# Kernel optimization log

Hardware: AMD Instinct MI355X
Metric: run time of the kernel (lower is better)

Reference implementation:

```python
import jax, jax.numpy as jnp
import numpy as np

EMBED = 1024
HEADS = 16
HEAD_DIM = EMBED // HEADS
SCALE = HEAD_DIM ** -0.5


def setup_inputs() -> dict:
    key = jax.random.key(0)
    ks = jax.random.split(key, 5)
    B, N = 2, 2048
    x = jax.random.normal(ks[0], (B, N, EMBED), dtype=jnp.float32)
    # qkv Linear: weight [3*EMBED, EMBED], bias [3*EMBED]
    w_qkv = jax.random.normal(ks[1], (3 * EMBED, EMBED), dtype=jnp.float32) * (EMBED ** -0.5)
    b_qkv = jnp.zeros((3 * EMBED,), dtype=jnp.float32)
    # proj Linear: weight [EMBED, EMBED], bias [EMBED]
    w_proj = jax.random.normal(ks[2], (EMBED, EMBED), dtype=jnp.float32) * (EMBED ** -0.5)
    b_proj = jnp.zeros((EMBED,), dtype=jnp.float32)
    return {"x": x, "w_qkv": w_qkv, "b_qkv": b_qkv, "w_proj": w_proj, "b_proj": b_proj}


def reference(x, w_qkv, b_qkv, w_proj, b_proj):
    B, N, _ = x.shape
    # QKV projection: [B, N, 3*EMBED]
    qkv = jnp.einsum('bnc,dc->bnd', x, w_qkv) + b_qkv
    qkv = qkv.reshape(B, N, 3, HEADS, HEAD_DIM).transpose(2, 0, 3, 1, 4)  # [3, B, H, N, Dh]
    q, k, v = qkv[0], qkv[1], qkv[2]
    # Explicit attention: matmul -> scale -> softmax -> matmul (eval mode, no dropout)
    attn = jnp.einsum('bhqd,bhkd->bhqk', q, k) * SCALE
    attn = jax.nn.softmax(attn, axis=-1)
    out = jnp.einsum('bhqk,bhkd->bhqd', attn, v)
    out = out.transpose(0, 2, 1, 3).reshape(B, N, EMBED)
    # Output projection (gamma1 is Identity; dropouts are zero in eval)
    out = jnp.einsum('bnc,dc->bnd', out, w_proj) + b_proj
    return out
```

## Files before the change

### kernel.cpp

```cpp
#include <hip/hip_runtime.h>
#include <stdint.h>

#define SEQ 2048

typedef __attribute__((ext_vector_type(8))) short bf16x8;
typedef __attribute__((ext_vector_type(4))) float f32x4;

typedef const __attribute__((address_space(1))) unsigned int GVT;
typedef __attribute__((address_space(3))) unsigned int LVT;

static __device__ __forceinline__ unsigned short f2bf(float f) {
  unsigned u = __builtin_bit_cast(unsigned, f);
  u += 0x7fffu + ((u >> 16) & 1u);
  return (unsigned short)(u >> 16);
}

static __device__ __forceinline__ unsigned pk_bf16(float lo, float hi) {
  unsigned r;
  asm("v_cvt_pk_bf16_f32 %0, %1, %2" : "=v"(r) : "v"(lo), "v"(hi));
  return r;
}

__global__ __launch_bounds__(256) void cvt_kernel(const float* __restrict__ src,
                                                  unsigned short* __restrict__ dst, int n4) {
  int i = blockIdx.x * 256 + threadIdx.x;
  const int stride = gridDim.x * 256;
  for (; i < n4; i += stride) {
    float4 v = reinterpret_cast<const float4*>(src)[i];
    ushort4 o;
    o.x = f2bf(v.x); o.y = f2bf(v.y); o.z = f2bf(v.z); o.w = f2bf(v.w);
    reinterpret_cast<ushort4*>(dst)[i] = o;
  }
}

__global__ __launch_bounds__(256, 2) void gemm_qkv_kernel(
    const unsigned short* __restrict__ A,
    const unsigned short* __restrict__ Bt,
    const float* __restrict__ bias,
    unsigned short* __restrict__ qb,
    unsigned short* __restrict__ kbuf,
    unsigned short* __restrict__ vtbuf) {
  __shared__ __align__(16) unsigned short As[2][128 * 32];
  __shared__ __align__(16) unsigned short Bs[2][128 * 32];
  const int tid = threadIdx.x;
  const int lane = tid & 63;
  const int wid = tid >> 6;
  const int wr = wid >> 1, wc = wid & 1;
  const int bm = blockIdx.y, bn = blockIdx.x;
  const int lr = lane & 15, hg = lane >> 4;

  f32x4 acc[4][4] = {};

  const int r0 = tid >> 2;
  const int c0 = (tid & 3) * 8;

  auto STAGE = [&](int b, int kt) {
    const unsigned short* ga0 = A + (size_t)(bm * 128 + r0) * 1024 + kt * 32 + c0;
    const unsigned short* ga1 = A + (size_t)(bm * 128 + r0 + 64) * 1024 + kt * 32 + c0;
    const unsigned short* gb0 = Bt + (size_t)(bn * 128 + r0) * 1024 + kt * 32 + c0;
    const unsigned short* gb1 = Bt + (size_t)(bn * 128 + r0 + 64) * 1024 + kt * 32 + c0;
    __builtin_amdgcn_global_load_lds((GVT*)ga0, (LVT*)&As[b][tid * 8], 16, 0, 0);
    __builtin_amdgcn_global_load_lds((GVT*)ga1, (LVT*)&As[b][(tid + 256) * 8], 16, 0, 0);
    __builtin_amdgcn_global_load_lds((GVT*)gb0, (LVT*)&Bs[b][tid * 8], 16, 0, 0);
    __builtin_amdgcn_global_load_lds((GVT*)gb1, (LVT*)&Bs[b][(tid + 256) * 8], 16, 0, 0);
  };

  STAGE(0, 0);
  int cur = 0;
  for (int kt = 0; kt < 32; ++kt) {
    __syncthreads();
    if (kt + 1 < 32) STAGE(cur ^ 1, kt + 1);
    bf16x8 af[4], bfr[4];
#pragma unroll
    for (int i = 0; i < 4; ++i) {
      af[i] = *reinterpret_cast<const bf16x8*>(&As[cur][(wr * 64 + i * 16 + lr) * 32 + hg * 8]);
      bfr[i] = *reinterpret_cast<const bf16x8*>(&Bs[cur][(wc * 64 + i * 16 + lr) * 32 + hg * 8]);
    }
#pragma unroll
    for (int i = 0; i < 4; ++i)
#pragma unroll
      for (int j = 0; j < 4; ++j)
        acc[i][j] = __builtin_amdgcn_mfma_f32_16x16x32_bf16(af[i], bfr[j], acc[i][j], 0, 0, 0);
    cur ^= 1;
  }

#pragma unroll
  for (int j = 0; j < 4; ++j) {
    const int col = bn * 128 + wc * 64 + j * 16 + lr;
    const float bv = bias[col];
    const int which = col >> 10;
    const int hh = (col >> 6) & 15;
    const int dh = col & 63;
    const float scl = which == 0 ? 0.18033688011112042f : 1.0f;
#pragma unroll
    for (int i = 0; i < 4; ++i) {
      if (which == 2) {
        const int row0 = bm * 128 + wr * 64 + i * 16 + hg * 4;
        const int b = row0 >> 11, n0 = row0 & 2047;
        ushort4 vv;
        vv.x = f2bf(acc[i][j][0] + bv);
        vv.y = f2bf(acc[i][j][1] + bv);
        vv.z = f2bf(acc[i][j][2] + bv);
        vv.w = f2bf(acc[i][j][3] + bv);
        *reinterpret_cast<ushort4*>(
            &vtbuf[((size_t)((b * 16 + hh) * 64 + dh)) * 2048 + n0]) = vv;
      } else {
        unsigned short* dst = which == 0 ? qb : kbuf;
#pragma unroll
        for (int r = 0; r < 4; ++r) {
          const int row = bm * 128 + wr * 64 + i * 16 + hg * 4 + r;
          const int b = row >> 11, n = row & 2047;
          dst[((size_t)((b * 16 + hh) * 2048 + n)) * 64 + dh] = f2bf((acc[i][j][r] + bv) * scl);
        }
      }
    }
  }
}

__global__ __launch_bounds__(256, 2) void gemm_proj_kernel(
    const unsigned short* __restrict__ A,
    const unsigned short* __restrict__ Bt,
    const float* __restrict__ bias,
    float* __restrict__ out) {
  __shared__ __align__(16) unsigned short As[2][128 * 32];
  __shared__ __align__(16) unsigned short Bs[2][128 * 32];
  const int tid = threadIdx.x;
  const int lane = tid & 63;
  const int wid = tid >> 6;
  const int wr = wid >> 1, wc = wid & 1;
  const int bm = blockIdx.y, bn = blockIdx.x;
  const int lr = lane & 15, hg = lane >> 4;

  f32x4 acc[4][4] = {};
  const int r0 = tid >> 2;
  const int c0 = (tid & 3) * 8;

  auto STAGE = [&](int b, int kt) {
    const unsigned short* ga0 = A + (size_t)(bm * 128 + r0) * 1024 + kt * 32 + c0;
    const unsigned short* ga1 = A + (size_t)(bm * 128 + r0 + 64) * 1024 + kt * 32 + c0;
    const unsigned short* gb0 = Bt + (size_t)(bn * 128 + r0) * 1024 + kt * 32 + c0;
    const unsigned short* gb1 = Bt + (size_t)(bn * 128 + r0 + 64) * 1024 + kt * 32 + c0;
    __builtin_amdgcn_global_load_lds((GVT*)ga0, (LVT*)&As[b][tid * 8], 16, 0, 0);
    __builtin_amdgcn_global_load_lds((GVT*)ga1, (LVT*)&As[b][(tid + 256) * 8], 16, 0, 0);
    __builtin_amdgcn_global_load_lds((GVT*)gb0, (LVT*)&Bs[b][tid * 8], 16, 0, 0);
    __builtin_amdgcn_global_load_lds((GVT*)gb1, (LVT*)&Bs[b][(tid + 256) * 8], 16, 0, 0);
  };

  STAGE(0, 0);
  int cur = 0;
  for (int kt = 0; kt < 32; ++kt) {
    __syncthreads();
    if (kt + 1 < 32) STAGE(cur ^ 1, kt + 1);
    bf16x8 af[4], bfr[4];
#pragma unroll
    for (int i = 0; i < 4; ++i) {
      af[i] = *reinterpret_cast<const bf16x8*>(&As[cur][(wr * 64 + i * 16 + lr) * 32 + hg * 8]);
      bfr[i] = *reinterpret_cast<const bf16x8*>(&Bs[cur][(wc * 64 + i * 16 + lr) * 32 + hg * 8]);
    }
#pragma unroll
    for (int i = 0; i < 4; ++i)
#pragma unroll
      for (int j = 0; j < 4; ++j)
        acc[i][j] = __builtin_amdgcn_mfma_f32_16x16x32_bf16(af[i], bfr[j], acc[i][j], 0, 0, 0);
    cur ^= 1;
  }

#pragma unroll
  for (int j = 0; j < 4; ++j) {
    const int col = bn * 128 + wc * 64 + j * 16 + lr;
    const float bv = bias[col];
#pragma unroll
    for (int i = 0; i < 4; ++i)
#pragma unroll
      for (int r = 0; r < 4; ++r) {
        const int row = bm * 128 + wr * 64 + i * 16 + hg * 4 + r;
        out[(size_t)row * 1024 + col] = acc[i][j][r] + bv;
      }
  }
}

__global__ __launch_bounds__(256, 2) void attn_kernel(
    const unsigned short* __restrict__ qb,
    const unsigned short* __restrict__ kbuf,
    const unsigned short* __restrict__ vt,
    unsigned short* __restrict__ ao) {
  __shared__ __align__(16) unsigned short Ks[2][64 * 64];
  __shared__ __align__(16) unsigned short Vs[2][64 * 64];
  __shared__ __align__(16) unsigned short Ps[4][32][88];
  const int tid = threadIdx.x;
  const int lane = tid & 63;
  const int wid = tid >> 6;
  const int lr = lane & 15;
  const int hg = lane >> 4;
  const int lin = blockIdx.y * 16 + blockIdx.x;
  const int wg = (lin & 7) * 64 + (lin >> 3);
  const int qt = wg & 15;
  const int bh = wg >> 4;
  const size_t hbase = (size_t)bh * SEQ * 64;

  bf16x8 qf[2][2];
#pragma unroll
  for (int m = 0; m < 2; ++m) {
    const unsigned short* qp =
        qb + hbase + (size_t)(qt * 128 + wid * 32 + m * 16 + lr) * 64 + hg * 8;
    qf[m][0] = *reinterpret_cast<const bf16x8*>(qp);
    qf[m][1] = *reinterpret_cast<const bf16x8*>(qp + 32);
  }

  f32x4 accO[2][4] = {};
  float m_run[2] = {-1e30f, -1e30f};
  float l_run[2] = {0.0f, 0.0f};

  auto STAGE = [&](int b, int kt) {
#pragma unroll
    for (int c = 0; c < 2; ++c) {
      const int t = tid + c * 256;
      const int row = t >> 3;
      const int sw = ((t & 7) ^ (row & 7)) * 8;
      const unsigned short* gk = kbuf + hbase + (size_t)(kt * 64 + row) * 64 + sw;
      __builtin_amdgcn_global_load_lds((GVT*)gk, (LVT*)&Ks[b][t * 8], 16, 0, 0);
      const unsigned short* gv = vt + hbase + (size_t)row * 2048 + kt * 64 + sw;
      __builtin_amdgcn_global_load_lds((GVT*)gv, (LVT*)&Vs[b][t * 8], 16, 0, 0);
    }
  };

  STAGE(0, 0);
  int cur = 0;
  const int sw0 = (hg ^ (lr & 7)) * 8;
  const int sw1 = ((hg + 4) ^ (lr & 7)) * 8;

  for (int kt = 0; kt < 32; ++kt) {
    __syncthreads();
    if (kt + 1 < 32) STAGE(cur ^ 1, kt + 1);

    f32x4 accT[2][4] = {};
#pragma unroll
    for (int j = 0; j < 4; ++j) {
      const bf16x8 kf0 = *reinterpret_cast<const bf16x8*>(&Ks[cur][(j * 16 + lr) * 64 + sw0]);
      const bf16x8 kf1 = *reinterpret_cast<const bf16x8*>(&Ks[cur][(j * 16 + lr) * 64 + sw1]);
      accT[0][j] = __builtin_amdgcn_mfma_f32_16x16x32_bf16(kf0, qf[0][0], accT[0][j], 0, 0, 0);
      accT[0][j] = __builtin_amdgcn_mfma_f32_16x16x32_bf16(kf1, qf[0][1], accT[0][j], 0, 0, 0);
      accT[1][j] = __builtin_amdgcn_mfma_f32_16x16x32_bf16(kf0, qf[1][0], accT[1][j], 0, 0, 0);
      accT[1][j] = __builtin_amdgcn_mfma_f32_16x16x32_bf16(kf1, qf[1][1], accT[1][j], 0, 0, 0);
    }

#pragma unroll
    for (int m = 0; m < 2; ++m) {
      float mt = accT[m][0][0];
#pragma unroll
      for (int j = 0; j < 4; ++j)
#pragma unroll
        for (int r = 0; r < 4; ++r) mt = fmaxf(mt, accT[m][j][r]);
      mt = fmaxf(mt, __shfl_xor(mt, 16));
      mt = fmaxf(mt, __shfl_xor(mt, 32));
      if (__any(mt > m_run[m] + 8.0f)) {
        const float mnew = fmaxf(m_run[m], mt);
        const float crr = __builtin_amdgcn_exp2f(m_run[m] - mnew);
        m_run[m] = mnew;
        l_run[m] *= crr;
#pragma unroll
        for (int jd = 0; jd < 4; ++jd)
#pragma unroll
          for (int r = 0; r < 4; ++r) accO[m][jd][r] *= crr;
      }
      float ps = 0.0f;
#pragma unroll
      for (int j = 0; j < 4; ++j) {
        const float p0 = __builtin_amdgcn_exp2f(accT[m][j][0] - m_run[m]);
        const float p1 = __builtin_amdgcn_exp2f(accT[m][j][1] - m_run[m]);
        const float p2 = __builtin_amdgcn_exp2f(accT[m][j][2] - m_run[m]);
        const float p3 = __builtin_amdgcn_exp2f(accT[m][j][3] - m_run[m]);
        ps += (p0 + p1) + (p2 + p3);
        uint2 w;
        w.x = pk_bf16(p0, p1);
        w.y = pk_bf16(p2, p3);
        *reinterpret_cast<uint2*>(&Ps[wid][m * 16 + lr][j * 16 + hg * 4]) = w;
      }
      ps += __shfl_xor(ps, 16);
      ps += __shfl_xor(ps, 32);
      l_run[m] += ps;
    }

    bf16x8 pB[2][2];
#pragma unroll
    for (int m = 0; m < 2; ++m) {
      pB[m][0] = *reinterpret_cast<const bf16x8*>(&Ps[wid][m * 16 + lr][hg * 8]);
      pB[m][1] = *reinterpret_cast<const bf16x8*>(&Ps[wid][m * 16 + lr][32 + hg * 8]);
    }
#pragma unroll
    for (int jd = 0; jd < 4; ++jd) {
      const bf16x8 v0 = *reinterpret_cast<const bf16x8*>(&Vs[cur][(jd * 16 + lr) * 64 + sw0]);
      const bf16x8 v1 = *reinterpret_cast<const bf16x8*>(&Vs[cur][(jd * 16 + lr) * 64 + sw1]);
      accO[0][jd] = __builtin_amdgcn_mfma_f32_16x16x32_bf16(v0, pB[0][0], accO[0][jd], 0, 0, 0);
      accO[0][jd] = __builtin_amdgcn_mfma_f32_16x16x32_bf16(v1, pB[0][1], accO[0][jd], 0, 0, 0);
      accO[1][jd] = __builtin_amdgcn_mfma_f32_16x16x32_bf16(v0, pB[1][0], accO[1][jd], 0, 0, 0);
      accO[1][jd] = __builtin_amdgcn_mfma_f32_16x16x32_bf16(v1, pB[1][1], accO[1][jd], 0, 0, 0);
    }
    cur ^= 1;
  }

  const int b = bh >> 4, hh = bh & 15;
#pragma unroll
  for (int m = 0; m < 2; ++m) {
    const float invl = 1.0f / l_run[m];
    const int qrow = qt * 128 + wid * 32 + m * 16 + lr;
    unsigned short* dst = ao + (size_t)(b * 2048 + qrow) * 1024 + hh * 64;
#pragma unroll
    for (int jd = 0; jd < 4; ++jd) {
      uint2 o;
      o.x = pk_bf16(accO[m][jd][0] * invl, accO[m][jd][1] * invl);
      o.y = pk_bf16(accO[m][jd][2] * invl, accO[m][jd][3] * invl);
      *reinterpret_cast<uint2*>(dst + jd * 16 + hg * 4) = o;
    }
  }
}

extern "C" void kernel_launch(void* const* d_in, const int* in_sizes, int n_in,
                              void* d_out, int out_size, void* d_ws, size_t ws_size,
                              hipStream_t stream) {
  const float* x = (const float*)d_in[0];
  const float* w_qkv = (const float*)d_in[1];
  const float* b_qkv = (const float*)d_in[2];
  const float* w_proj = (const float*)d_in[3];
  const float* b_proj = (const float*)d_in[4];
  float* out = (float*)d_out;
  char* ws = (char*)d_ws;
  unsigned short* x_bf = (unsigned short*)(ws);
  unsigned short* ao_bf = (unsigned short*)(ws);
  unsigned short* wq_bf = (unsigned short*)(ws + (8ull << 20));
  unsigned short* wp_bf = (unsigned short*)(ws + (14ull << 20));
  unsigned short* q_bf = (unsigned short*)(ws + (16ull << 20));
  unsigned short* k_bf = (unsigned short*)(ws + (24ull << 20));
  unsigned short* vt_bf = (unsigned short*)(ws + (32ull << 20));

  cvt_kernel<<<1024, 256, 0, stream>>>(x, x_bf, 4096 * 1024 / 4);
  cvt_kernel<<<1024, 256, 0, stream>>>(w_qkv, wq_bf, 3072 * 1024 / 4);
  cvt_kernel<<<512, 256, 0, stream>>>(w_proj, wp_bf, 1024 * 1024 / 4);
  gemm_qkv_kernel<<<dim3(24, 32), 256, 0, stream>>>(x_bf, wq_bf, b_qkv, q_bf, k_bf, vt_bf);
  attn_kernel<<<dim3(16, 32), 256, 0, stream>>>(q_bf, k_bf, vt_bf, ao_bf);
  gemm_proj_kernel<<<dim3(8, 32), 256, 0, stream>>>(ao_bf, wp_bf, b_proj, out);
}
```

Baseline: 136.5 us.

## Fuse conversion kernels, remap GEMM tiles, and load attention K/V directly into registers

Merges the three fp32-to-bf16 conversion launches into one kernel. Remaps GEMM workgroup indices with an XCD-aware swizzle to improve L2 locality. Raises wave priority around the MFMA blocks with s_setprio. The attention kernel drops its LDS K/V staging: each wave reads its K and V fragments straight from global memory into registers, prefetching the next tile, and the max reduction is restructured into a tree. This removes barriers and LDS traffic, but every wave now loads K/V separately from global/L2 instead of sharing them through LDS.

```diff
diff --git a/kernel.cpp b/kernel.cpp
--- a/kernel.cpp
+++ b/kernel.cpp
@@ -21,15 +21,24 @@
   return r;
 }
 
-__global__ __launch_bounds__(256) void cvt_kernel(const float* __restrict__ src,
-                                                  unsigned short* __restrict__ dst, int n4) {
+__global__ __launch_bounds__(256) void cvt3_kernel(
+    const float* __restrict__ s0, unsigned short* __restrict__ d0, int n0,
+    const float* __restrict__ s1, unsigned short* __restrict__ d1, int n1,
+    const float* __restrict__ s2, unsigned short* __restrict__ d2, int n2) {
   int i = blockIdx.x * 256 + threadIdx.x;
   const int stride = gridDim.x * 256;
-  for (; i < n4; i += stride) {
-    float4 v = reinterpret_cast<const float4*>(src)[i];
+  const int total = n0 + n1 + n2;
+  for (; i < total; i += stride) {
+    const float* s;
+    unsigned short* d;
+    int k;
+    if (i < n0) { s = s0; d = d0; k = i; }
+    else if (i < n0 + n1) { s = s1; d = d1; k = i - n0; }
+    else { s = s2; d = d2; k = i - n0 - n1; }
+    float4 v = reinterpret_cast<const float4*>(s)[k];
     ushort4 o;
     o.x = f2bf(v.x); o.y = f2bf(v.y); o.z = f2bf(v.z); o.w = f2bf(v.w);
-    reinterpret_cast<ushort4*>(dst)[i] = o;
+    reinterpret_cast<ushort4*>(d)[k] = o;
   }
 }
 
@@ -46,7 +55,9 @@
   const int lane = tid & 63;
   const int wid = tid >> 6;
   const int wr = wid >> 1, wc = wid & 1;
-  const int bm = blockIdx.y, bn = blockIdx.x;
+  const int lin = blockIdx.y * 24 + blockIdx.x;
+  const int wg = (lin & 7) * 96 + (lin >> 3);
+  const int bm = wg / 24, bn = wg % 24;
   const int lr = lane & 15, hg = lane >> 4;
 
   f32x4 acc[4][4] = {};
@@ -76,11 +87,13 @@
       af[i] = *reinterpret_cast<const bf16x8*>(&As[cur][(wr * 64 + i * 16 + lr) * 32 + hg * 8]);
       bfr[i] = *reinterpret_cast<const bf16x8*>(&Bs[cur][(wc * 64 + i * 16 + lr) * 32 + hg * 8]);
     }
+    __builtin_amdgcn_s_setprio(1);
 #pragma unroll
     for (int i = 0; i < 4; ++i)
 #pragma unroll
       for (int j = 0; j < 4; ++j)
         acc[i][j] = __builtin_amdgcn_mfma_f32_16x16x32_bf16(af[i], bfr[j], acc[i][j], 0, 0, 0);
+    __builtin_amdgcn_s_setprio(0);
     cur ^= 1;
   }
 
@@ -128,7 +141,9 @@
   const int lane = tid & 63;
   const int wid = tid >> 6;
   const int wr = wid >> 1, wc = wid & 1;
-  const int bm = blockIdx.y, bn = blockIdx.x;
+  const int lin = blockIdx.y * 8 + blockIdx.x;
+  const int wg = (lin & 7) * 32 + (lin >> 3);
+  const int bm = wg / 8, bn = wg % 8;
   const int lr = lane & 15, hg = lane >> 4;
 
   f32x4 acc[4][4] = {};
@@ -157,11 +172,13 @@
       af[i] = *reinterpret_cast<const bf16x8*>(&As[cur][(wr * 64 + i * 16 + lr) * 32 + hg * 8]);
       bfr[i] = *reinterpret_cast<const bf16x8*>(&Bs[cur][(wc * 64 + i * 16 + lr) * 32 + hg * 8]);
     }
+    __builtin_amdgcn_s_setprio(1);
 #pragma unroll
     for (int i = 0; i < 4; ++i)
 #pragma unroll
       for (int j = 0; j < 4; ++j)
         acc[i][j] = __builtin_amdgcn_mfma_f32_16x16x32_bf16(af[i], bfr[j], acc[i][j], 0, 0, 0);
+    __builtin_amdgcn_s_setprio(0);
     cur ^= 1;
   }
 
@@ -184,8 +201,6 @@
     const unsigned short* __restrict__ kbuf,
     const unsigned short* __restrict__ vt,
     unsigned short* __restrict__ ao) {
-  __shared__ __align__(16) unsigned short Ks[2][64 * 64];
-  __shared__ __align__(16) unsigned short Vs[2][64 * 64];
   __shared__ __align__(16) unsigned short Ps[4][32][88];
   const int tid = threadIdx.x;
   const int lane = tid & 63;
@@ -207,50 +222,49 @@
     qf[m][1] = *reinterpret_cast<const bf16x8*>(qp + 32);
   }
 
+  bf16x8 kf[4][2];
+  bf16x8 vf[4][2];
+  const unsigned short* kb0 = kbuf + hbase + (size_t)(lr)*64 + hg * 8;
+  const unsigned short* vb0 = vt + hbase + (size_t)(lr)*2048 + hg * 8;
+#pragma unroll
+  for (int j = 0; j < 4; ++j) {
+    kf[j][0] = *reinterpret_cast<const bf16x8*>(kb0 + (size_t)(j * 16) * 64);
+    kf[j][1] = *reinterpret_cast<const bf16x8*>(kb0 + (size_t)(j * 16) * 64 + 32);
+    vf[j][0] = *reinterpret_cast<const bf16x8*>(vb0 + (size_t)(j * 16) * 2048);
+    vf[j][1] = *reinterpret_cast<const bf16x8*>(vb0 + (size_t)(j * 16) * 2048 + 32);
+  }
+
   f32x4 accO[2][4] = {};
   float m_run[2] = {-1e30f, -1e30f};
   float l_run[2] = {0.0f, 0.0f};
 
-  auto STAGE = [&](int b, int kt) {
-#pragma unroll
-    for (int c = 0; c < 2; ++c) {
-      const int t = tid + c * 256;
-      const int row = t >> 3;
-      const int sw = ((t & 7) ^ (row & 7)) * 8;
-      const unsigned short* gk = kbuf + hbase + (size_t)(kt * 64 + row) * 64 + sw;
-      __builtin_amdgcn_global_load_lds((GVT*)gk, (LVT*)&Ks[b][t * 8], 16, 0, 0);
-      const unsigned short* gv = vt + hbase + (size_t)row * 2048 + kt * 64 + sw;
-      __builtin_amdgcn_global_load_lds((GVT*)gv, (LVT*)&Vs[b][t * 8], 16, 0, 0);
-    }
-  };
-
-  STAGE(0, 0);
-  int cur = 0;
-  const int sw0 = (hg ^ (lr & 7)) * 8;
-  const int sw1 = ((hg + 4) ^ (lr & 7)) * 8;
-
   for (int kt = 0; kt < 32; ++kt) {
-    __syncthreads();
-    if (kt + 1 < 32) STAGE(cur ^ 1, kt + 1);
+    const int ktn = kt < 31 ? kt + 1 : 31;
 
     f32x4 accT[2][4] = {};
+    __builtin_amdgcn_s_setprio(1);
 #pragma unroll
     for (int j = 0; j < 4; ++j) {
-      const bf16x8 kf0 = *reinterpret_cast<const bf16x8*>(&Ks[cur][(j * 16 + lr) * 64 + sw0]);
-      const bf16x8 kf1 = *reinterpret_cast<const bf16x8*>(&Ks[cur][(j * 16 + lr) * 64 + sw1]);
-      accT[0][j] = __builtin_amdgcn_mfma_f32_16x16x32_bf16(kf0, qf[0][0], accT[0][j], 0, 0, 0);
-      accT[0][j] = __builtin_amdgcn_mfma_f32_16x16x32_bf16(kf1, qf[0][1], accT[0][j], 0, 0, 0);
-      accT[1][j] = __builtin_amdgcn_mfma_f32_16x16x32_bf16(kf0, qf[1][0], accT[1][j], 0, 0, 0);
-      accT[1][j] = __builtin_amdgcn_mfma_f32_16x16x32_bf16(kf1, qf[1][1], accT[1][j], 0, 0, 0);
+      accT[0][j] = __builtin_amdgcn_mfma_f32_16x16x32_bf16(kf[j][0], qf[0][0], accT[0][j], 0, 0, 0);
+      accT[0][j] = __builtin_amdgcn_mfma_f32_16x16x32_bf16(kf[j][1], qf[0][1], accT[0][j], 0, 0, 0);
+      accT[1][j] = __builtin_amdgcn_mfma_f32_16x16x32_bf16(kf[j][0], qf[1][0], accT[1][j], 0, 0, 0);
+      accT[1][j] = __builtin_amdgcn_mfma_f32_16x16x32_bf16(kf[j][1], qf[1][1], accT[1][j], 0, 0, 0);
+    }
+    __builtin_amdgcn_s_setprio(0);
+
+#pragma unroll
+    for (int j = 0; j < 4; ++j) {
+      kf[j][0] = *reinterpret_cast<const bf16x8*>(kb0 + (size_t)(ktn * 64 + j * 16) * 64);
+      kf[j][1] = *reinterpret_cast<const bf16x8*>(kb0 + (size_t)(ktn * 64 + j * 16) * 64 + 32);
     }
 
 #pragma unroll
     for (int m = 0; m < 2; ++m) {
-      float mt = accT[m][0][0];
-#pragma unroll
-      for (int j = 0; j < 4; ++j)
-#pragma unroll
-        for (int r = 0; r < 4; ++r) mt = fmaxf(mt, accT[m][j][r]);
+      float t0 = fmaxf(fmaxf(accT[m][0][0], accT[m][0][1]), fmaxf(accT[m][0][2], accT[m][0][3]));
+      float t1 = fmaxf(fmaxf(accT[m][1][0], accT[m][1][1]), fmaxf(accT[m][1][2], accT[m][1][3]));
+      float t2 = fmaxf(fmaxf(accT[m][2][0], accT[m][2][1]), fmaxf(accT[m][2][2], accT[m][2][3]));
+      float t3 = fmaxf(fmaxf(accT[m][3][0], accT[m][3][1]), fmaxf(accT[m][3][2], accT[m][3][3]));
+      float mt = fmaxf(fmaxf(t0, t1), fmaxf(t2, t3));
       mt = fmaxf(mt, __shfl_xor(mt, 16));
       mt = fmaxf(mt, __shfl_xor(mt, 32));
       if (__any(mt > m_run[m] + 8.0f)) {
@@ -263,19 +277,21 @@
 #pragma unroll
           for (int r = 0; r < 4; ++r) accO[m][jd][r] *= crr;
       }
-      float ps = 0.0f;
+      float ps0 = 0.f, ps1 = 0.f;
 #pragma unroll
       for (int j = 0; j < 4; ++j) {
         const float p0 = __builtin_amdgcn_exp2f(accT[m][j][0] - m_run[m]);
         const float p1 = __builtin_amdgcn_exp2f(accT[m][j][1] - m_run[m]);
         const float p2 = __builtin_amdgcn_exp2f(accT[m][j][2] - m_run[m]);
         const float p3 = __builtin_amdgcn_exp2f(accT[m][j][3] - m_run[m]);
-        ps += (p0 + p1) + (p2 + p3);
+        ps0 += (p0 + p1);
+        ps1 += (p2 + p3);
         uint2 w;
         w.x = pk_bf16(p0, p1);
         w.y = pk_bf16(p2, p3);
         *reinterpret_cast<uint2*>(&Ps[wid][m * 16 + lr][j * 16 + hg * 4]) = w;
       }
+      float ps = ps0 + ps1;
       ps += __shfl_xor(ps, 16);
       ps += __shfl_xor(ps, 32);
       l_run[m] += ps;
@@ -287,16 +303,21 @@
       pB[m][0] = *reinterpret_cast<const bf16x8*>(&Ps[wid][m * 16 + lr][hg * 8]);
       pB[m][1] = *reinterpret_cast<const bf16x8*>(&Ps[wid][m * 16 + lr][32 + hg * 8]);
     }
+    __builtin_amdgcn_s_setprio(1);
 #pragma unroll
     for (int jd = 0; jd < 4; ++jd) {
-      const bf16x8 v0 = *reinterpret_cast<const bf16x8*>(&Vs[cur][(jd * 16 + lr) * 64 + sw0]);
-      const bf16x8 v1 = *reinterpret_cast<const bf16x8*>(&Vs[cur][(jd * 16 + lr) * 64 + sw1]);
-      accO[0][jd] = __builtin_amdgcn_mfma_f32_16x16x32_bf16(v0, pB[0][0], accO[0][jd], 0, 0, 0);
-      accO[0][jd] = __builtin_amdgcn_mfma_f32_16x16x32_bf16(v1, pB[0][1], accO[0][jd], 0, 0, 0);
-      accO[1][jd] = __builtin_amdgcn_mfma_f32_16x16x32_bf16(v0, pB[1][0], accO[1][jd], 0, 0, 0);
-      accO[1][jd] = __builtin_amdgcn_mfma_f32_16x16x32_bf16(v1, pB[1][1], accO[1][jd], 0, 0, 0);
-    }
-    cur ^= 1;
+      accO[0][jd] = __builtin_amdgcn_mfma_f32_16x16x32_bf16(vf[jd][0], pB[0][0], accO[0][jd], 0, 0, 0);
+      accO[0][jd] = __builtin_amdgcn_mfma_f32_16x16x32_bf16(vf[jd][1], pB[0][1], accO[0][jd], 0, 0, 0);
+      accO[1][jd] = __builtin_amdgcn_mfma_f32_16x16x32_bf16(vf[jd][0], pB[1][0], accO[1][jd], 0, 0, 0);
+      accO[1][jd] = __builtin_amdgcn_mfma_f32_16x16x32_bf16(vf[jd][1], pB[1][1], accO[1][jd], 0, 0, 0);
+    }
+    __builtin_amdgcn_s_setprio(0);
+
+#pragma unroll
+    for (int jd = 0; jd < 4; ++jd) {
+      vf[jd][0] = *reinterpret_cast<const bf16x8*>(vb0 + (size_t)(jd * 16) * 2048 + ktn * 64);
+      vf[jd][1] = *reinterpret_cast<const bf16x8*>(vb0 + (size_t)(jd * 16) * 2048 + ktn * 64 + 32);
+    }
   }
 
   const int b = bh >> 4, hh = bh & 15;
@@ -333,9 +354,9 @@
   unsigned short* k_bf = (unsigned short*)(ws + (24ull << 20));
   unsigned short* vt_bf = (unsigned short*)(ws + (32ull << 20));
 
-  cvt_kernel<<<1024, 256, 0, stream>>>(x, x_bf, 4096 * 1024 / 4);
-  cvt_kernel<<<1024, 256, 0, stream>>>(w_qkv, wq_bf, 3072 * 1024 / 4);
-  cvt_kernel<<<512, 256, 0, stream>>>(w_proj, wp_bf, 1024 * 1024 / 4);
+  cvt3_kernel<<<2048, 256, 0, stream>>>(x, x_bf, 4096 * 1024 / 4,
+                                        w_qkv, wq_bf, 3072 * 1024 / 4,
+                                        w_proj, wp_bf, 1024 * 1024 / 4);
   gemm_qkv_kernel<<<dim3(24, 32), 256, 0, stream>>>(x_bf, wq_bf, b_qkv, q_bf, k_bf, vt_bf);
   attn_kernel<<<dim3(16, 32), 256, 0, stream>>>(q_bf, k_bf, vt_bf, ao_bf);
   gemm_proj_kernel<<<dim3(8, 32), 256, 0, stream>>>(ao_bf, wp_bf, b_proj, out);
```

Result: slower. 184.9 us (+35.5%).

## Fuse conversions, remap GEMM blocks, add setprio, and pass P via permlane swaps

Applied to the files above, without the earlier changes.

The three fp32-to-bf16 conversion launches become a single kernel. Both GEMMs remap block indices so consecutive workgroups spread across XCDs. s_setprio is raised around the MFMA bursts in the GEMMs and the attention kernel. The attention kernel drops the shared-memory round trip for the P tile and instead rearranges packed bf16 probabilities across lanes with v_permlane32/16_swap, which removes LDS writes and reads but depends on the lane mapping being exactly right.

```diff
diff --git a/kernel.cpp b/kernel.cpp
--- a/kernel.cpp
+++ b/kernel.cpp
@@ -5,6 +5,7 @@
 
 typedef __attribute__((ext_vector_type(8))) short bf16x8;
 typedef __attribute__((ext_vector_type(4))) float f32x4;
+typedef __attribute__((ext_vector_type(4))) int i32x4;
 
 typedef const __attribute__((address_space(1))) unsigned int GVT;
 typedef __attribute__((address_space(3))) unsigned int LVT;
@@ -21,15 +22,24 @@
   return r;
 }
 
-__global__ __launch_bounds__(256) void cvt_kernel(const float* __restrict__ src,
-                                                  unsigned short* __restrict__ dst, int n4) {
+__global__ __launch_bounds__(256) void cvt3_kernel(
+    const float* __restrict__ s0, unsigned short* __restrict__ d0, int n0,
+    const float* __restrict__ s1, unsigned short* __restrict__ d1, int n1,
+    const float* __restrict__ s2, unsigned short* __restrict__ d2, int n2) {
   int i = blockIdx.x * 256 + threadIdx.x;
   const int stride = gridDim.x * 256;
-  for (; i < n4; i += stride) {
-    float4 v = reinterpret_cast<const float4*>(src)[i];
+  const int total = n0 + n1 + n2;
+  for (; i < total; i += stride) {
+    const float* s;
+    unsigned short* d;
+    int k;
+    if (i < n0) { s = s0; d = d0; k = i; }
+    else if (i < n0 + n1) { s = s1; d = d1; k = i - n0; }
+    else { s = s2; d = d2; k = i - n0 - n1; }
+    float4 v = reinterpret_cast<const float4*>(s)[k];
     ushort4 o;
     o.x = f2bf(v.x); o.y = f2bf(v.y); o.z = f2bf(v.z); o.w = f2bf(v.w);
-    reinterpret_cast<ushort4*>(dst)[i] = o;
+    reinterpret_cast<ushort4*>(d)[k] = o;
   }
 }
 
@@ -46,7 +56,9 @@
   const int lane = tid & 63;
   const int wid = tid >> 6;
   const int wr = wid >> 1, wc = wid & 1;
-  const int bm = blockIdx.y, bn = blockIdx.x;
+  const int lin = blockIdx.y * 24 + blockIdx.x;
+  const int wg = (lin & 7) * 96 + (lin >> 3);
+  const int bm = wg / 24, bn = wg % 24;
   const int lr = lane & 15, hg = lane >> 4;
 
   f32x4 acc[4][4] = {};
@@ -76,11 +88,13 @@
       af[i] = *reinterpret_cast<const bf16x8*>(&As[cur][(wr * 64 + i * 16 + lr) * 32 + hg * 8]);
       bfr[i] = *reinterpret_cast<const bf16x8*>(&Bs[cur][(wc * 64 + i * 16 + lr) * 32 + hg * 8]);
     }
+    __builtin_amdgcn_s_setprio(1);
 #pragma unroll
     for (int i = 0; i < 4; ++i)
 #pragma unroll
       for (int j = 0; j < 4; ++j)
         acc[i][j] = __builtin_amdgcn_mfma_f32_16x16x32_bf16(af[i], bfr[j], acc[i][j], 0, 0, 0);
+    __builtin_amdgcn_s_setprio(0);
     cur ^= 1;
   }
 
@@ -128,7 +142,9 @@
   const int lane = tid & 63;
   const int wid = tid >> 6;
   const int wr = wid >> 1, wc = wid & 1;
-  const int bm = blockIdx.y, bn = blockIdx.x;
+  const int lin = blockIdx.y * 8 + blockIdx.x;
+  const int wg = (lin & 7) * 32 + (lin >> 3);
+  const int bm = wg / 8, bn = wg % 8;
   const int lr = lane & 15, hg = lane >> 4;
 
   f32x4 acc[4][4] = {};
@@ -157,11 +173,13 @@
       af[i] = *reinterpret_cast<const bf16x8*>(&As[cur][(wr * 64 + i * 16 + lr) * 32 + hg * 8]);
       bfr[i] = *reinterpret_cast<const bf16x8*>(&Bs[cur][(wc * 64 + i * 16 + lr) * 32 + hg * 8]);
     }
+    __builtin_amdgcn_s_setprio(1);
 #pragma unroll
     for (int i = 0; i < 4; ++i)
 #pragma unroll
       for (int j = 0; j < 4; ++j)
         acc[i][j] = __builtin_amdgcn_mfma_f32_16x16x32_bf16(af[i], bfr[j], acc[i][j], 0, 0, 0);
+    __builtin_amdgcn_s_setprio(0);
     cur ^= 1;
   }
 
@@ -186,7 +204,6 @@
     unsigned short* __restrict__ ao) {
   __shared__ __align__(16) unsigned short Ks[2][64 * 64];
   __shared__ __align__(16) unsigned short Vs[2][64 * 64];
-  __shared__ __align__(16) unsigned short Ps[4][32][88];
   const int tid = threadIdx.x;
   const int lane = tid & 63;
   const int wid = tid >> 6;
@@ -234,6 +251,7 @@
     if (kt + 1 < 32) STAGE(cur ^ 1, kt + 1);
 
     f32x4 accT[2][4] = {};
+    __builtin_amdgcn_s_setprio(1);
 #pragma unroll
     for (int j = 0; j < 4; ++j) {
       const bf16x8 kf0 = *reinterpret_cast<const bf16x8*>(&Ks[cur][(j * 16 + lr) * 64 + sw0]);
@@ -243,14 +261,16 @@
       accT[1][j] = __builtin_amdgcn_mfma_f32_16x16x32_bf16(kf0, qf[1][0], accT[1][j], 0, 0, 0);
       accT[1][j] = __builtin_amdgcn_mfma_f32_16x16x32_bf16(kf1, qf[1][1], accT[1][j], 0, 0, 0);
     }
-
+    __builtin_amdgcn_s_setprio(0);
+
+    bf16x8 pB[2][2];
 #pragma unroll
     for (int m = 0; m < 2; ++m) {
-      float mt = accT[m][0][0];
-#pragma unroll
-      for (int j = 0; j < 4; ++j)
-#pragma unroll
-        for (int r = 0; r < 4; ++r) mt = fmaxf(mt, accT[m][j][r]);
+      float t0 = fmaxf(fmaxf(accT[m][0][0], accT[m][0][1]), fmaxf(accT[m][0][2], accT[m][0][3]));
+      float t1 = fmaxf(fmaxf(accT[m][1][0], accT[m][1][1]), fmaxf(accT[m][1][2], accT[m][1][3]));
+      float t2 = fmaxf(fmaxf(accT[m][2][0], accT[m][2][1]), fmaxf(accT[m][2][2], accT[m][2][3]));
+      float t3 = fmaxf(fmaxf(accT[m][3][0], accT[m][3][1]), fmaxf(accT[m][3][2], accT[m][3][3]));
+      float mt = fmaxf(fmaxf(t0, t1), fmaxf(t2, t3));
       mt = fmaxf(mt, __shfl_xor(mt, 16));
       mt = fmaxf(mt, __shfl_xor(mt, 32));
       if (__any(mt > m_run[m] + 8.0f)) {
@@ -263,30 +283,37 @@
 #pragma unroll
           for (int r = 0; r < 4; ++r) accO[m][jd][r] *= crr;
       }
-      float ps = 0.0f;
+      unsigned w[4][2];
+      float ps0 = 0.f, ps1 = 0.f;
 #pragma unroll
       for (int j = 0; j < 4; ++j) {
         const float p0 = __builtin_amdgcn_exp2f(accT[m][j][0] - m_run[m]);
         const float p1 = __builtin_amdgcn_exp2f(accT[m][j][1] - m_run[m]);
         const float p2 = __builtin_amdgcn_exp2f(accT[m][j][2] - m_run[m]);
         const float p3 = __builtin_amdgcn_exp2f(accT[m][j][3] - m_run[m]);
-        ps += (p0 + p1) + (p2 + p3);
-        uint2 w;
-        w.x = pk_bf16(p0, p1);
-        w.y = pk_bf16(p2, p3);
-        *reinterpret_cast<uint2*>(&Ps[wid][m * 16 + lr][j * 16 + hg * 4]) = w;
-      }
+        ps0 += (p0 + p1);
+        ps1 += (p2 + p3);
+        w[j][0] = pk_bf16(p0, p1);
+        w[j][1] = pk_bf16(p2, p3);
+      }
+      float ps = ps0 + ps1;
       ps += __shfl_xor(ps, 16);
       ps += __shfl_xor(ps, 32);
       l_run[m] += ps;
-    }
-
-    bf16x8 pB[2][2];
-#pragma unroll
-    for (int m = 0; m < 2; ++m) {
-      pB[m][0] = *reinterpret_cast<const bf16x8*>(&Ps[wid][m * 16 + lr][hg * 8]);
-      pB[m][1] = *reinterpret_cast<const bf16x8*>(&Ps[wid][m * 16 + lr][32 + hg * 8]);
-    }
+#pragma unroll
+      for (int h = 0; h < 2; ++h) {
+        unsigned e0 = w[2 * h][0], e1 = w[2 * h][1];
+        unsigned f0 = w[2 * h + 1][0], f1 = w[2 * h + 1][1];
+        asm("v_permlane32_swap_b32 %0, %1" : "+v"(e0), "+v"(f0));
+        asm("v_permlane32_swap_b32 %0, %1" : "+v"(e1), "+v"(f1));
+        asm("v_permlane16_swap_b32 %0, %1" : "+v"(e0), "+v"(f0));
+        asm("v_permlane16_swap_b32 %0, %1" : "+v"(e1), "+v"(f1));
+        const i32x4 pw = {(int)e0, (int)e1, (int)f0, (int)f1};
+        pB[m][h] = __builtin_bit_cast(bf16x8, pw);
+      }
+    }
+
+    __builtin_amdgcn_s_setprio(1);
 #pragma unroll
     for (int jd = 0; jd < 4; ++jd) {
       const bf16x8 v0 = *reinterpret_cast<const bf16x8*>(&Vs[cur][(jd * 16 + lr) * 64 + sw0]);
@@ -296,6 +323,7 @@
       accO[1][jd] = __builtin_amdgcn_mfma_f32_16x16x32_bf16(v0, pB[1][0], accO[1][jd], 0, 0, 0);
       accO[1][jd] = __builtin_amdgcn_mfma_f32_16x16x32_bf16(v1, pB[1][1], accO[1][jd], 0, 0, 0);
     }
+    __builtin_amdgcn_s_setprio(0);
     cur ^= 1;
   }
 
@@ -333,9 +361,9 @@
   unsigned short* k_bf = (unsigned short*)(ws + (24ull << 20));
   unsigned short* vt_bf = (unsigned short*)(ws + (32ull << 20));
 
-  cvt_kernel<<<1024, 256, 0, stream>>>(x, x_bf, 4096 * 1024 / 4);
-  cvt_kernel<<<1024, 256, 0, stream>>>(w_qkv, wq_bf, 3072 * 1024 / 4);
-  cvt_kernel<<<512, 256, 0, stream>>>(w_proj, wp_bf, 1024 * 1024 / 4);
+  cvt3_kernel<<<2048, 256, 0, stream>>>(x, x_bf, 4096 * 1024 / 4,
+                                        w_qkv, wq_bf, 3072 * 1024 / 4,
+                                        w_proj, wp_bf, 1024 * 1024 / 4);
   gemm_qkv_kernel<<<dim3(24, 32), 256, 0, stream>>>(x_bf, wq_bf, b_qkv, q_bf, k_bf, vt_bf);
   attn_kernel<<<dim3(16, 32), 256, 0, stream>>>(q_bf, k_bf, vt_bf, ao_bf);
   gemm_proj_kernel<<<dim3(8, 32), 256, 0, stream>>>(ao_bf, wp_bf, b_proj, out);
```

New measurement: 130.4 us. 4.4% less time.
